# Optimization experiments

Measured on AMD Instinct MI355X. Metric: run time of the kernel, lower is better.

The kernel has to match this reference:

```python
import jax, jax.numpy as jnp
from jax import lax
import numpy as np

DG = 2          # deformable groups
KH = KW = 3     # kernel size
KK = KH * KW
PAD = 1


def setup_inputs() -> dict:
    key = jax.random.key(0)
    k1, k2, k3 = jax.random.split(key, 3)
    B, C, H, W = 4, 64, 128, 128
    O = 64
    x = jax.random.normal(k1, (B, C, H, W), jnp.float32)
    # original inits offset weights to 0 (degenerate: plain conv); use small random
    # weights instead so the irregular bilinear-gather path is actually exercised.
    w_off = jax.random.normal(k2, (DG * 2 * KK, C, KH, KW), jnp.float32) * 0.05
    w_def = jax.random.normal(k3, (O, C, KH, KW), jnp.float32) * (1.0 / np.sqrt(C * KK))
    return {"x": x, "w_off": w_off, "w_def": w_def}


def _deform_conv(x, w_off, w_def):
    B, C, H, W = x.shape
    O = w_def.shape[0]
    Cg = C // DG

    # offset = offset_conv(x): stride 1, pad 1, no bias -> [B, DG*2*KK, H, W]
    offset = lax.conv_general_dilated(
        x, w_off, window_strides=(1, 1), padding=((PAD, PAD), (PAD, PAD)),
        dimension_numbers=("NCHW", "OIHW", "NCHW"))
    # DCN layout: per group, per kernel tap k, channel 2k = dy, 2k+1 = dx
    off = offset.reshape(B, DG, KK, 2, H, W)

    ki, kj = jnp.meshgrid(jnp.arange(KH), jnp.arange(KW), indexing="ij")
    ki = (ki.reshape(KK) - PAD).astype(x.dtype)   # kernel row offsets -1..1
    kj = (kj.reshape(KK) - PAD).astype(x.dtype)
    hh = jnp.arange(H, dtype=x.dtype)
    ww = jnp.arange(W, dtype=x.dtype)

    # sampling positions [B, DG, KK, H, W]
    py = off[:, :, :, 0] + ki[None, None, :, None, None] + hh[None, None, None, :, None]
    px = off[:, :, :, 1] + kj[None, None, :, None, None] + ww[None, None, None, None, :]

    y0 = jnp.floor(py).astype(jnp.int32)
    x0 = jnp.floor(px).astype(jnp.int32)
    dy = py - y0.astype(x.dtype)
    dx = px - x0.astype(x.dtype)

    x_g = x.reshape(B, DG, Cg, H * W)

    def gather(yi, xi):
        # zero padding outside the image
        valid = ((yi >= 0) & (yi < H) & (xi >= 0) & (xi < W)).astype(x.dtype)
        yc = jnp.clip(yi, 0, H - 1)
        xc = jnp.clip(xi, 0, W - 1)
        idx = (yc * W + xc).reshape(B, DG, 1, KK * H * W)
        v = jnp.take_along_axis(x_g, idx, axis=3).reshape(B, DG, Cg, KK, H, W)
        return v * valid[:, :, None]  # broadcast over channel axis

    # bilinear interpolation at learned offset positions
    val = (gather(y0, x0) * ((1 - dy) * (1 - dx))[:, :, None]
           + gather(y0, x0 + 1) * ((1 - dy) * dx)[:, :, None]
           + gather(y0 + 1, x0) * (dy * (1 - dx))[:, :, None]
           + gather(y0 + 1, x0 + 1) * (dy * dx)[:, :, None])

    # weighted accumulation: conv groups = 1, channel dim = DG*Cg
    w = w_def.reshape(O, DG, Cg, KK)
    return jnp.einsum("bgckhw,ogck->bohw", val, w)


def reference(x, w_off, w_def):
    return _deform_conv(x, w_off, w_def)
```

## Files before the change

### kernel.cpp

```cpp
#include <hip/hip_runtime.h>
#include <hip/hip_bf16.h>

typedef _Float16 f16x8 __attribute__((ext_vector_type(8)));
typedef _Float16 f16x2 __attribute__((ext_vector_type(2)));
typedef float f32x4  __attribute__((ext_vector_type(4)));

#define Bn 4
#define Cn 64
#define Hn 128
#define Wn 128
#define HWn 16384

#define XT_BYTES    (Bn*HWn*Cn*2)
#define PKDEF_BYTES (18*4*64*8*2)

static __device__ __forceinline__ unsigned pk_f16(float lo, float hi) {
  union { _Float16 h[2]; unsigned u; } cv;
  cv.h[0] = (_Float16)lo; cv.h[1] = (_Float16)hi;
  return cv.u;
}

__global__ __launch_bounds__(256) void prep_all(const float* __restrict__ x,
                                                const float* __restrict__ w_off,
                                                const float* __restrict__ w_def,
                                                ushort* __restrict__ xt,
                                                ushort* __restrict__ pk_def,
                                                ushort* __restrict__ pk_off) {
  __shared__ float tile[64][68];
  const int t = threadIdx.x;
  const int blk = blockIdx.x;
  if (blk < 1024) {
    const int b = blk >> 8;
    const int pix0 = (blk & 255) * 64;
    const int y = pix0 >> 7, x0 = pix0 & 127;
    const float* xb = x + (b * Cn) * HWn + pix0;
#pragma unroll
    for (int q = 0; q < 4; ++q) {
      int idx = q * 256 + t;
      int c = idx >> 4, p4 = idx & 15;
      float4 v = *(const float4*)(xb + c * HWn + p4 * 4);
      *(float4*)&tile[c][p4 * 4] = v;
    }
    __syncthreads();
    const int p = t & 63, cg = t >> 6;
#pragma unroll
    for (int half = 0; half < 2; ++half) {
      const int seg = cg * 2 + half;
      unsigned u[4];
#pragma unroll
      for (int j = 0; j < 4; ++j)
        u[j] = pk_f16(tile[seg * 8 + 2 * j][p], tile[seg * 8 + 2 * j + 1][p]);
      uint4 v = {u[0], u[1], u[2], u[3]};
      *(uint4*)(xt + (((((b << 7) + y) << 3) + seg) * 128 + x0 + p) * 8) = v;
    }
  } else {
    const int tt = (blk - 1024) * 256 + t;
    if (tt < 4608) {
      int lane = tt & 63, oc = (tt >> 6) & 3, s = tt >> 8;
      int g = s / 9, k = s % 9;
      int o = oc * 16 + (lane & 15);
      int cb = g * 32 + (lane >> 4) * 8;
      unsigned u[4];
#pragma unroll
      for (int j = 0; j < 4; ++j)
        u[j] = pk_f16(w_def[(o * Cn + cb + 2 * j) * 9 + k],
                      w_def[(o * Cn + cb + 2 * j + 1) * 9 + k]);
      uint4 v = {u[0], u[1], u[2], u[3]};
      *(uint4*)(pk_def + tt * 8) = v;
    } else if (tt < 8064) {
      int t2 = tt - 4608;
      int lane = t2 & 63, r = t2 >> 6;
      int oc = r % 3, s = r / 3;
      int k = s >> 1, chalf = s & 1;
      int o = oc * 16 + (lane & 15);
      int cb = chalf * 32 + (lane >> 4) * 8;
      unsigned u[4];
#pragma unroll
      for (int j = 0; j < 4; ++j) {
        float lo = (o < 36) ? w_off[(o * Cn + cb + 2 * j) * 9 + k] : 0.f;
        float hi = (o < 36) ? w_off[(o * Cn + cb + 2 * j + 1) * 9 + k] : 0.f;
        u[j] = pk_f16(lo, hi);
      }
      uint4 v = {u[0], u[1], u[2], u[3]};
      *(uint4*)(pk_off + (r * 64 + lane) * 8) = v;
    }
  }
}

#define T_STRIDE (17*24*8 + 16)
__global__ __launch_bounds__(1024, 4) void deform_fused(const ushort* __restrict__ xt,
                                                        const ushort* __restrict__ pk_def,
                                                        const ushort* __restrict__ pk_off,
                                                        float* __restrict__ out) {
  __shared__ ushort tile[8 * T_STRIDE];
  __shared__ _Float16 off_lds[8][36][18];
  const int t = threadIdx.x;
  const int lane = t & 63;
  const int wid = t >> 6;
  const int pg = wid >> 1, gsel = wid & 1;
  int bid = blockIdx.x;
  bid = (bid & 7) * 64 + (bid >> 3);
  const int b  = bid >> 7;
  const int ty = (bid >> 3) & 15;
  const int tx = bid & 7;
  const int y0t = ty * 8, x0t = tx * 16;
  const int TLY = max(0, y0t - 4), THY = min(127, y0t + 12);
  const int TLX = max(0, x0t - 3), THX = min(127, x0t + 19);
  const int Hd = THY - TLY + 1, Wd = THX - TLX + 1;

  {
    const int xq = t & 31;
    const int r0 = t >> 5;
    const int nr = Hd * 8;
    for (int rr = r0; rr < nr; rr += 32) {
      const int yq = rr >> 3, seg = rr & 7;
      if (xq < Wd) {
        const ushort* src = xt + ((((b << 7) + TLY + yq) << 3) + seg) * 1024 + (TLX + xq) * 8;
        *(uint4*)&tile[seg * T_STRIDE + (yq * 24 + xq) * 8] = *(const uint4*)src;
      }
    }
  }
  __syncthreads();

  const int h = y0t + pg;
  const int p = lane & 15, kq = lane >> 4;
  const int w_ = x0t + p;
  const int pixin = (h << 7) + x0t;
  const int su = gsel * 4 + kq;
  const int colb = lane & 15;

  int pixoff[9]; bool tvalid[9];
#pragma unroll
  for (int kk = 0; kk < 9; ++kk) {
    int yk = h + kk / 3 - 1, xk = w_ + kk % 3 - 1;
    tvalid[kk] = ((unsigned)yk < 128u) && ((unsigned)xk < 128u);
    int yc = min(max(yk, 0), 127), xc = min(max(xk, 0), 127);
    pixoff[kk] = ((yc - TLY) * 24 + (xc - TLX)) * 8;
  }

  {
    f32x4 oa0 = {0,0,0,0}, oa1 = {0,0,0,0}, oa2 = {0,0,0,0};
    const f16x8* pBo = (const f16x8*)pk_off;
    f16x8 bo[2][2];
    if (gsel == 0) bo[0][0] = pBo[0*64 + lane];
    else { bo[0][0] = pBo[1*64 + lane]; bo[0][1] = pBo[2*64 + lane]; }
#pragma unroll
    for (int s = 0; s < 18; ++s) {
      if (s + 1 < 18) {
        if (gsel == 0) bo[(s + 1) & 1][0] = pBo[((s + 1)*3 + 0)*64 + lane];
        else { bo[(s + 1) & 1][0] = pBo[((s + 1)*3 + 1)*64 + lane];
               bo[(s + 1) & 1][1] = pBo[((s + 1)*3 + 2)*64 + lane]; }
      }
      const int k = s >> 1, chalf = s & 1;
      uint4 t_ = *(const uint4*)&tile[(chalf * 4 + kq) * T_STRIDE + pixoff[k]];
      if (!tvalid[k]) { t_.x = 0; t_.y = 0; t_.z = 0; t_.w = 0; }
      union { uint4 u; f16x8 v; } A; A.u = t_;
      if (gsel == 0) {
        oa0 = __builtin_amdgcn_mfma_f32_16x16x32_f16(A.v, bo[s & 1][0], oa0, 0,0,0);
      } else {
        oa1 = __builtin_amdgcn_mfma_f32_16x16x32_f16(A.v, bo[s & 1][0], oa1, 0,0,0);
        oa2 = __builtin_amdgcn_mfma_f32_16x16x32_f16(A.v, bo[s & 1][1], oa2, 0,0,0);
      }
    }
    if (gsel == 0) {
#pragma unroll
      for (int r = 0; r < 4; ++r) off_lds[pg][colb][kq * 4 + r] = (_Float16)oa0[r];
    } else {
#pragma unroll
      for (int r = 0; r < 4; ++r) {
        off_lds[pg][16 + colb][kq * 4 + r] = (_Float16)oa1[r];
        if (colb < 4) off_lds[pg][32 + colb][kq * 4 + r] = (_Float16)oa2[r];
      }
    }
  }
  __syncthreads();

  float offv[18];
#pragma unroll
  for (int j = 0; j < 18; ++j) offv[j] = (float)off_lds[pg][gsel * 18 + j][p];

  f32x4 acc0={0,0,0,0}, acc1={0,0,0,0}, acc2={0,0,0,0}, acc3={0,0,0,0};
  const f16x8* pB = (const f16x8*)pk_def;

  f16x8 bq[2][4];
  {
    const int s0 = gsel * 9;
#pragma unroll
    for (int q = 0; q < 4; ++q) bq[0][q] = pB[(s0*4 + q)*64 + lane];
  }

#pragma unroll
  for (int j = 0; j < 9; ++j) {
    if (j + 1 < 9) {
      const int s1 = gsel * 9 + j + 1;
#pragma unroll
      for (int q = 0; q < 4; ++q) bq[(j + 1) & 1][q] = pB[(s1*4 + q)*64 + lane];
    }

    const int k = j;
    float py = offv[2*j]   + (float)(h  + k / 3 - 1);
    float px = offv[2*j+1] + (float)(w_ + k % 3 - 1);
    float fy = floorf(py), fx = floorf(px);
    int y0 = (int)fy, x0 = (int)fx;
    float dy = py - fy, dx = px - fx;

    bool vy0 = (y0 >= 0) && (y0 < Hn);
    bool vy1 = (y0 >= -1) && (y0 < Hn - 1);
    bool vx0 = (x0 >= 0) && (x0 < Wn);
    bool vx1 = (x0 >= -1) && (x0 < Wn - 1);
    float omdy = 1.f - dy, omdx = 1.f - dx;
    float w00 = (vy0 && vx0) ? omdy * omdx : 0.f;
    float w01 = (vy0 && vx1) ? omdy * dx   : 0.f;
    float w10 = (vy1 && vx0) ? dy * omdx   : 0.f;
    float w11 = (vy1 && vx1) ? dy * dx     : 0.f;

    int iy0 = min(max(y0, 0), Hn - 1), iy1 = min(max(y0 + 1, 0), Hn - 1);
    int ix0 = min(max(x0, 0), Wn - 1), ix1 = min(max(x0 + 1, 0), Wn - 1);

    uint4 c00, c01, c10, c11;
    bool intile = (iy0 >= TLY) && (iy1 <= THY) && (ix0 >= TLX) && (ix1 <= THX);
    if (__all((int)intile)) {
      const int base = su * T_STRIDE;
      const int ly0 = iy0 - TLY, ly1 = iy1 - TLY;
      const int lx0 = ix0 - TLX, lx1 = ix1 - TLX;
      c00 = *(const uint4*)&tile[base + (ly0 * 24 + lx0) * 8];
      c01 = *(const uint4*)&tile[base + (ly0 * 24 + lx1) * 8];
      c10 = *(const uint4*)&tile[base + (ly1 * 24 + lx0) * 8];
      c11 = *(const uint4*)&tile[base + (ly1 * 24 + lx1) * 8];
    } else {
      const int r0g = ((((b << 7) + iy0) << 3) + su) * 128;
      const int r1g = ((((b << 7) + iy1) << 3) + su) * 128;
      c00 = *(const uint4*)(xt + (r0g + ix0) * 8);
      c01 = *(const uint4*)(xt + (r0g + ix1) * 8);
      c10 = *(const uint4*)(xt + (r1g + ix0) * 8);
      c11 = *(const uint4*)(xt + (r1g + ix1) * 8);
    }

    const _Float16 h00 = (_Float16)w00, h01 = (_Float16)w01;
    const _Float16 h10 = (_Float16)w10, h11 = (_Float16)w11;
    const f16x2 W00 = {h00, h00}, W01 = {h01, h01};
    const f16x2 W10 = {h10, h10}, W11 = {h11, h11};
    union U32H { unsigned u; f16x2 h; };
    union { uint4 u; f16x8 v; } A;
#define BILC(comp, fld)                                                        \
    { U32H a0, a1, a2, a3, r;                                                  \
      a0.u = c00.comp; a1.u = c01.comp; a2.u = c10.comp; a3.u = c11.comp;      \
      r.h = a0.h * W00 + a1.h * W01 + a2.h * W10 + a3.h * W11;                 \
      A.u.fld = r.u; }
    BILC(x, x) BILC(y, y) BILC(z, z) BILC(w, w)
#undef BILC

    acc0 = __builtin_amdgcn_mfma_f32_16x16x32_f16(A.v, bq[j & 1][0], acc0, 0,0,0);
    acc1 = __builtin_amdgcn_mfma_f32_16x16x32_f16(A.v, bq[j & 1][1], acc1, 0,0,0);
    acc2 = __builtin_amdgcn_mfma_f32_16x16x32_f16(A.v, bq[j & 1][2], acc2, 0,0,0);
    acc3 = __builtin_amdgcn_mfma_f32_16x16x32_f16(A.v, bq[j & 1][3], acc3, 0,0,0);
  }

  __syncthreads();
  float* red = (float*)tile;
  if (gsel == 1) {
    *(f32x4*)&red[((pg * 4 + 0) * 64 + lane) * 4] = acc0;
    *(f32x4*)&red[((pg * 4 + 1) * 64 + lane) * 4] = acc1;
  } else {
    *(f32x4*)&red[((pg * 4 + 2) * 64 + lane) * 4] = acc2;
    *(f32x4*)&red[((pg * 4 + 3) * 64 + lane) * 4] = acc3;
  }
  __syncthreads();
  float* ob = out + pixin + kq * 4;
  if (gsel == 0) {
    acc0 += *(const f32x4*)&red[((pg * 4 + 0) * 64 + lane) * 4];
    acc1 += *(const f32x4*)&red[((pg * 4 + 1) * 64 + lane) * 4];
#pragma unroll
    for (int r = 0; r < 4; ++r) {
      ob[((b*64 +      colb) << 14) + r] = acc0[r];
      ob[((b*64 + 16 + colb) << 14) + r] = acc1[r];
    }
  } else {
    acc2 += *(const f32x4*)&red[((pg * 4 + 2) * 64 + lane) * 4];
    acc3 += *(const f32x4*)&red[((pg * 4 + 3) * 64 + lane) * 4];
#pragma unroll
    for (int r = 0; r < 4; ++r) {
      ob[((b*64 + 32 + colb) << 14) + r] = acc2[r];
      ob[((b*64 + 48 + colb) << 14) + r] = acc3[r];
    }
  }
}

extern "C" void kernel_launch(void* const* d_in, const int* in_sizes, int n_in,
                              void* d_out, int out_size, void* d_ws, size_t ws_size,
                              hipStream_t stream) {
  const float* x     = (const float*)d_in[0];
  const float* w_off = (const float*)d_in[1];
  const float* w_def = (const float*)d_in[2];
  float* out = (float*)d_out;

  char* ws = (char*)d_ws;
  ushort* xt     = (ushort*)ws;
  ushort* pk_def = (ushort*)(ws + XT_BYTES);
  ushort* pk_off = (ushort*)(ws + XT_BYTES + PKDEF_BYTES);

  prep_all<<<1056, 256, 0, stream>>>(x, w_off, w_def, xt, pk_def, pk_off);
  deform_fused<<<512, 1024, 0, stream>>>(xt, pk_def, pk_off, out);
}
```

Measured before the change: 55.00 us.

## Process two row tiles per block with double-buffered async LDS staging

Each block now handles two vertically adjacent 8-row tiles, halving the grid. The second tile's halo is staged into a second LDS buffer with global_load_lds while the first tile's bilinear/MFMA phase runs. The intent is to hide tile-load latency behind compute and reuse per-block setup. The cost is fewer blocks and more LDS per block, which may reduce parallelism on a 256-CU device.

```diff
diff --git a/kernel.cpp b/kernel.cpp
--- a/kernel.cpp
+++ b/kernel.cpp
@@ -14,10 +14,19 @@
 #define XT_BYTES    (Bn*HWn*Cn*2)
 #define PKDEF_BYTES (18*4*64*8*2)
 
+#define T_STRIDE (17*25*8)
+#define TILE_USH (8*T_STRIDE)
+
 static __device__ __forceinline__ unsigned pk_f16(float lo, float hi) {
   union { _Float16 h[2]; unsigned u; } cv;
   cv.h[0] = (_Float16)lo; cv.h[1] = (_Float16)hi;
   return cv.u;
+}
+
+static __device__ __forceinline__ void gload16(const ushort* g, ushort* l) {
+  __builtin_amdgcn_global_load_lds(
+      (const __attribute__((address_space(1))) void*)g,
+      (__attribute__((address_space(3))) void*)l, 16, 0, 0);
 }
 
 __global__ __launch_bounds__(256) void prep_all(const float* __restrict__ x,
@@ -87,60 +96,62 @@
   }
 }
 
-#define T_STRIDE (17*24*8 + 16)
 __global__ __launch_bounds__(1024, 4) void deform_fused(const ushort* __restrict__ xt,
                                                         const ushort* __restrict__ pk_def,
                                                         const ushort* __restrict__ pk_off,
                                                         float* __restrict__ out) {
-  __shared__ ushort tile[8 * T_STRIDE];
+  __shared__ __align__(16) ushort tA[TILE_USH];
+  __shared__ __align__(16) ushort tB[TILE_USH];
   __shared__ _Float16 off_lds[8][36][18];
   const int t = threadIdx.x;
   const int lane = t & 63;
   const int wid = t >> 6;
   const int pg = wid >> 1, gsel = wid & 1;
   int bid = blockIdx.x;
-  bid = (bid & 7) * 64 + (bid >> 3);
-  const int b  = bid >> 7;
-  const int ty = (bid >> 3) & 15;
-  const int tx = bid & 7;
-  const int y0t = ty * 8, x0t = tx * 16;
-  const int TLY = max(0, y0t - 4), THY = min(127, y0t + 12);
-  const int TLX = max(0, x0t - 3), THX = min(127, x0t + 19);
-  const int Hd = THY - TLY + 1, Wd = THX - TLX + 1;
-
-  {
-    const int xq = t & 31;
-    const int r0 = t >> 5;
-    const int nr = Hd * 8;
-    for (int rr = r0; rr < nr; rr += 32) {
-      const int yq = rr >> 3, seg = rr & 7;
-      if (xq < Wd) {
-        const ushort* src = xt + ((((b << 7) + TLY + yq) << 3) + seg) * 1024 + (TLX + xq) * 8;
-        *(uint4*)&tile[seg * T_STRIDE + (yq * 24 + xq) * 8] = *(const uint4*)src;
-      }
-    }
-  }
-  __syncthreads();
-
-  const int h = y0t + pg;
+  bid = (bid & 7) * 32 + (bid >> 3);
+  const int b   = bid >> 6;
+  const int typ = (bid >> 3) & 7;
+  const int tx  = bid & 7;
+  const int x0t = tx * 16;
+
   const int p = lane & 15, kq = lane >> 4;
   const int w_ = x0t + p;
-  const int pixin = (h << 7) + x0t;
   const int su = gsel * 4 + kq;
   const int colb = lane & 15;
-
-  int pixoff[9]; bool tvalid[9];
-#pragma unroll
-  for (int kk = 0; kk < 9; ++kk) {
-    int yk = h + kk / 3 - 1, xk = w_ + kk % 3 - 1;
-    tvalid[kk] = ((unsigned)yk < 128u) && ((unsigned)xk < 128u);
-    int yc = min(max(yk, 0), 127), xc = min(max(xk, 0), 127);
-    pixoff[kk] = ((yc - TLY) * 24 + (xc - TLX)) * 8;
-  }
-
-  {
+  const f16x8* pB  = (const f16x8*)pk_def;
+  const f16x8* pBo = (const f16x8*)pk_off;
+
+  auto stage = [&](ushort* tbuf, int y0t) {
+    const int TLY = max(0, y0t - 4);
+    const int TLX = max(0, x0t - 4);
+    for (int base = wid * 64; base < 3400; base += 1024) {
+      int fi = base + lane;
+      if (fi < 3400) {
+        int seg = fi / 425;
+        int r   = fi - seg * 425;
+        int yq  = r / 25;
+        int xq  = r - yq * 25;
+        int gy = min(TLY + yq, 127);
+        int gx = min(TLX + xq, 127);
+        const ushort* src = xt + ((((b << 7) + gy) << 3) + seg) * 1024 + gx * 8;
+        gload16(src, tbuf + base * 8);
+      }
+    }
+  };
+
+  auto P1 = [&](const ushort* tbuf, int y0t) {
+    const int TLY = max(0, y0t - 4);
+    const int TLX = max(0, x0t - 4);
+    const int h = y0t + pg;
+    int pixoff[9]; bool tvalid[9];
+#pragma unroll
+    for (int kk = 0; kk < 9; ++kk) {
+      int yk = h + kk / 3 - 1, xk = w_ + kk % 3 - 1;
+      tvalid[kk] = ((unsigned)yk < 128u) && ((unsigned)xk < 128u);
+      int yc = min(max(yk, 0), 127), xc = min(max(xk, 0), 127);
+      pixoff[kk] = ((yc - TLY) * 25 + (xc - TLX)) * 8;
+    }
     f32x4 oa0 = {0,0,0,0}, oa1 = {0,0,0,0}, oa2 = {0,0,0,0};
-    const f16x8* pBo = (const f16x8*)pk_off;
     f16x8 bo[2][2];
     if (gsel == 0) bo[0][0] = pBo[0*64 + lane];
     else { bo[0][0] = pBo[1*64 + lane]; bo[0][1] = pBo[2*64 + lane]; }
@@ -152,7 +163,7 @@
                bo[(s + 1) & 1][1] = pBo[((s + 1)*3 + 2)*64 + lane]; }
       }
       const int k = s >> 1, chalf = s & 1;
-      uint4 t_ = *(const uint4*)&tile[(chalf * 4 + kq) * T_STRIDE + pixoff[k]];
+      uint4 t_ = *(const uint4*)&tbuf[(chalf * 4 + kq) * T_STRIDE + pixoff[k]];
       if (!tvalid[k]) { t_.x = 0; t_.y = 0; t_.z = 0; t_.w = 0; }
       union { uint4 u; f16x8 v; } A; A.u = t_;
       if (gsel == 0) {
@@ -172,118 +183,135 @@
         if (colb < 4) off_lds[pg][32 + colb][kq * 4 + r] = (_Float16)oa2[r];
       }
     }
-  }
-  __syncthreads();
-
-  float offv[18];
-#pragma unroll
-  for (int j = 0; j < 18; ++j) offv[j] = (float)off_lds[pg][gsel * 18 + j][p];
-
-  f32x4 acc0={0,0,0,0}, acc1={0,0,0,0}, acc2={0,0,0,0}, acc3={0,0,0,0};
-  const f16x8* pB = (const f16x8*)pk_def;
-
-  f16x8 bq[2][4];
-  {
-    const int s0 = gsel * 9;
-#pragma unroll
-    for (int q = 0; q < 4; ++q) bq[0][q] = pB[(s0*4 + q)*64 + lane];
-  }
-
-#pragma unroll
-  for (int j = 0; j < 9; ++j) {
-    if (j + 1 < 9) {
-      const int s1 = gsel * 9 + j + 1;
-#pragma unroll
-      for (int q = 0; q < 4; ++q) bq[(j + 1) & 1][q] = pB[(s1*4 + q)*64 + lane];
-    }
-
-    const int k = j;
-    float py = offv[2*j]   + (float)(h  + k / 3 - 1);
-    float px = offv[2*j+1] + (float)(w_ + k % 3 - 1);
-    float fy = floorf(py), fx = floorf(px);
-    int y0 = (int)fy, x0 = (int)fx;
-    float dy = py - fy, dx = px - fx;
-
-    bool vy0 = (y0 >= 0) && (y0 < Hn);
-    bool vy1 = (y0 >= -1) && (y0 < Hn - 1);
-    bool vx0 = (x0 >= 0) && (x0 < Wn);
-    bool vx1 = (x0 >= -1) && (x0 < Wn - 1);
-    float omdy = 1.f - dy, omdx = 1.f - dx;
-    float w00 = (vy0 && vx0) ? omdy * omdx : 0.f;
-    float w01 = (vy0 && vx1) ? omdy * dx   : 0.f;
-    float w10 = (vy1 && vx0) ? dy * omdx   : 0.f;
-    float w11 = (vy1 && vx1) ? dy * dx     : 0.f;
-
-    int iy0 = min(max(y0, 0), Hn - 1), iy1 = min(max(y0 + 1, 0), Hn - 1);
-    int ix0 = min(max(x0, 0), Wn - 1), ix1 = min(max(x0 + 1, 0), Wn - 1);
-
-    uint4 c00, c01, c10, c11;
-    bool intile = (iy0 >= TLY) && (iy1 <= THY) && (ix0 >= TLX) && (ix1 <= THX);
-    if (__all((int)intile)) {
-      const int base = su * T_STRIDE;
-      const int ly0 = iy0 - TLY, ly1 = iy1 - TLY;
-      const int lx0 = ix0 - TLX, lx1 = ix1 - TLX;
-      c00 = *(const uint4*)&tile[base + (ly0 * 24 + lx0) * 8];
-      c01 = *(const uint4*)&tile[base + (ly0 * 24 + lx1) * 8];
-      c10 = *(const uint4*)&tile[base + (ly1 * 24 + lx0) * 8];
-      c11 = *(const uint4*)&tile[base + (ly1 * 24 + lx1) * 8];
+  };
+
+  f32x4 acc0, acc1, acc2, acc3;
+
+  auto P2 = [&](const ushort* tbuf, int y0t) {
+    const int TLY = max(0, y0t - 4), THY = min(127, y0t + 12);
+    const int TLX = max(0, x0t - 4), THX = min(127, x0t + 20);
+    const int h = y0t + pg;
+    float offv[18];
+#pragma unroll
+    for (int j = 0; j < 18; ++j) offv[j] = (float)off_lds[pg][gsel * 18 + j][p];
+    acc0 = (f32x4){0,0,0,0}; acc1 = (f32x4){0,0,0,0};
+    acc2 = (f32x4){0,0,0,0}; acc3 = (f32x4){0,0,0,0};
+    f16x8 bq[2][4];
+    {
+      const int s0 = gsel * 9;
+#pragma unroll
+      for (int q = 0; q < 4; ++q) bq[0][q] = pB[(s0*4 + q)*64 + lane];
+    }
+#pragma unroll
+    for (int j = 0; j < 9; ++j) {
+      if (j + 1 < 9) {
+        const int s1 = gsel * 9 + j + 1;
+#pragma unroll
+        for (int q = 0; q < 4; ++q) bq[(j + 1) & 1][q] = pB[(s1*4 + q)*64 + lane];
+      }
+      const int k = j;
+      float py = offv[2*j]   + (float)(h  + k / 3 - 1);
+      float px = offv[2*j+1] + (float)(w_ + k % 3 - 1);
+      float fy = floorf(py), fx = floorf(px);
+      int y0 = (int)fy, x0 = (int)fx;
+      float dy = py - fy, dx = px - fx;
+      bool vy0 = (y0 >= 0) && (y0 < Hn);
+      bool vy1 = (y0 >= -1) && (y0 < Hn - 1);
+      bool vx0 = (x0 >= 0) && (x0 < Wn);
+      bool vx1 = (x0 >= -1) && (x0 < Wn - 1);
+      float omdy = 1.f - dy, omdx = 1.f - dx;
+      float w00 = (vy0 && vx0) ? omdy * omdx : 0.f;
+      float w01 = (vy0 && vx1) ? omdy * dx   : 0.f;
+      float w10 = (vy1 && vx0) ? dy * omdx   : 0.f;
+      float w11 = (vy1 && vx1) ? dy * dx     : 0.f;
+      int iy0 = min(max(y0, 0), Hn - 1), iy1 = min(max(y0 + 1, 0), Hn - 1);
+      int ix0 = min(max(x0, 0), Wn - 1), ix1 = min(max(x0 + 1, 0), Wn - 1);
+      uint4 c00, c01, c10, c11;
+      bool intile = (iy0 >= TLY) && (iy1 <= THY) && (ix0 >= TLX) && (ix1 <= THX);
+      if (__all((int)intile)) {
+        const int base = su * T_STRIDE;
+        const int ly0 = iy0 - TLY, ly1 = iy1 - TLY;
+        const int lx0 = ix0 - TLX, lx1 = ix1 - TLX;
+        c00 = *(const uint4*)&tbuf[base + (ly0 * 25 + lx0) * 8];
+        c01 = *(const uint4*)&tbuf[base + (ly0 * 25 + lx1) * 8];
+        c10 = *(const uint4*)&tbuf[base + (ly1 * 25 + lx0) * 8];
+        c11 = *(const uint4*)&tbuf[base + (ly1 * 25 + lx1) * 8];
+      } else {
+        const int r0g = ((((b << 7) + iy0) << 3) + su) * 128;
+        const int r1g = ((((b << 7) + iy1) << 3) + su) * 128;
+        c00 = *(const uint4*)(xt + (r0g + ix0) * 8);
+        c01 = *(const uint4*)(xt + (r0g + ix1) * 8);
+        c10 = *(const uint4*)(xt + (r1g + ix0) * 8);
+        c11 = *(const uint4*)(xt + (r1g + ix1) * 8);
+      }
+      const _Float16 h00 = (_Float16)w00, h01 = (_Float16)w01;
+      const _Float16 h10 = (_Float16)w10, h11 = (_Float16)w11;
+      const f16x2 W00 = {h00, h00}, W01 = {h01, h01};
+      const f16x2 W10 = {h10, h10}, W11 = {h11, h11};
+      union U32H { unsigned u; f16x2 h; };
+      union { uint4 u; f16x8 v; } A;
+#define BILC(comp, fld)                                                        \
+      { U32H a0, a1, a2, a3, r;                                                \
+        a0.u = c00.comp; a1.u = c01.comp; a2.u = c10.comp; a3.u = c11.comp;    \
+        r.h = a0.h * W00 + a1.h * W01 + a2.h * W10 + a3.h * W11;               \
+        A.u.fld = r.u; }
+      BILC(x, x) BILC(y, y) BILC(z, z) BILC(w, w)
+#undef BILC
+      acc0 = __builtin_amdgcn_mfma_f32_16x16x32_f16(A.v, bq[j & 1][0], acc0, 0,0,0);
+      acc1 = __builtin_amdgcn_mfma_f32_16x16x32_f16(A.v, bq[j & 1][1], acc1, 0,0,0);
+      acc2 = __builtin_amdgcn_mfma_f32_16x16x32_f16(A.v, bq[j & 1][2], acc2, 0,0,0);
+      acc3 = __builtin_amdgcn_mfma_f32_16x16x32_f16(A.v, bq[j & 1][3], acc3, 0,0,0);
+    }
+  };
+
+  auto RW = [&](float* red, int y0t) {
+    const int h = y0t + pg;
+    const int pixin = (h << 7) + x0t;
+    if (gsel == 1) {
+      *(f32x4*)&red[((pg * 4 + 0) * 64 + lane) * 4] = acc0;
+      *(f32x4*)&red[((pg * 4 + 1) * 64 + lane) * 4] = acc1;
     } else {
-      const int r0g = ((((b << 7) + iy0) << 3) + su) * 128;
-      const int r1g = ((((b << 7) + iy1) << 3) + su) * 128;
-      c00 = *(const uint4*)(xt + (r0g + ix0) * 8);
-      c01 = *(const uint4*)(xt + (r0g + ix1) * 8);
-      c10 = *(const uint4*)(xt + (r1g + ix0) * 8);
-      c11 = *(const uint4*)(xt + (r1g + ix1) * 8);
-    }
-
-    const _Float16 h00 = (_Float16)w00, h01 = (_Float16)w01;
-    const _Float16 h10 = (_Float16)w10, h11 = (_Float16)w11;
-    const f16x2 W00 = {h00, h00}, W01 = {h01, h01};
-    const f16x2 W10 = {h10, h10}, W11 = {h11, h11};
-    union U32H { unsigned u; f16x2 h; };
-    union { uint4 u; f16x8 v; } A;
-#define BILC(comp, fld)                                                        \
-    { U32H a0, a1, a2, a3, r;                                                  \
-      a0.u = c00.comp; a1.u = c01.comp; a2.u = c10.comp; a3.u = c11.comp;      \
-      r.h = a0.h * W00 + a1.h * W01 + a2.h * W10 + a3.h * W11;                 \
-      A.u.fld = r.u; }
-    BILC(x, x) BILC(y, y) BILC(z, z) BILC(w, w)
-#undef BILC
-
-    acc0 = __builtin_amdgcn_mfma_f32_16x16x32_f16(A.v, bq[j & 1][0], acc0, 0,0,0);
-    acc1 = __builtin_amdgcn_mfma_f32_16x16x32_f16(A.v, bq[j & 1][1], acc1, 0,0,0);
-    acc2 = __builtin_amdgcn_mfma_f32_16x16x32_f16(A.v, bq[j & 1][2], acc2, 0,0,0);
-    acc3 = __builtin_amdgcn_mfma_f32_16x16x32_f16(A.v, bq[j & 1][3], acc3, 0,0,0);
-  }
-
-  __syncthreads();
-  float* red = (float*)tile;
-  if (gsel == 1) {
-    *(f32x4*)&red[((pg * 4 + 0) * 64 + lane) * 4] = acc0;
-    *(f32x4*)&red[((pg * 4 + 1) * 64 + lane) * 4] = acc1;
-  } else {
-    *(f32x4*)&red[((pg * 4 + 2) * 64 + lane) * 4] = acc2;
-    *(f32x4*)&red[((pg * 4 + 3) * 64 + lane) * 4] = acc3;
-  }
-  __syncthreads();
-  float* ob = out + pixin + kq * 4;
-  if (gsel == 0) {
-    acc0 += *(const f32x4*)&red[((pg * 4 + 0) * 64 + lane) * 4];
-    acc1 += *(const f32x4*)&red[((pg * 4 + 1) * 64 + lane) * 4];
-#pragma unroll
-    for (int r = 0; r < 4; ++r) {
-      ob[((b*64 +      colb) << 14) + r] = acc0[r];
-      ob[((b*64 + 16 + colb) << 14) + r] = acc1[r];
-    }
-  } else {
-    acc2 += *(const f32x4*)&red[((pg * 4 + 2) * 64 + lane) * 4];
-    acc3 += *(const f32x4*)&red[((pg * 4 + 3) * 64 + lane) * 4];
-#pragma unroll
-    for (int r = 0; r < 4; ++r) {
-      ob[((b*64 + 32 + colb) << 14) + r] = acc2[r];
-      ob[((b*64 + 48 + colb) << 14) + r] = acc3[r];
-    }
-  }
+      *(f32x4*)&red[((pg * 4 + 2) * 64 + lane) * 4] = acc2;
+      *(f32x4*)&red[((pg * 4 + 3) * 64 + lane) * 4] = acc3;
+    }
+    __syncthreads();
+    float* ob = out + pixin + kq * 4;
+    if (gsel == 0) {
+      acc0 += *(const f32x4*)&red[((pg * 4 + 0) * 64 + lane) * 4];
+      acc1 += *(const f32x4*)&red[((pg * 4 + 1) * 64 + lane) * 4];
+#pragma unroll
+      for (int r = 0; r < 4; ++r) {
+        ob[((b*64 +      colb) << 14) + r] = acc0[r];
+        ob[((b*64 + 16 + colb) << 14) + r] = acc1[r];
+      }
+    } else {
+      acc2 += *(const f32x4*)&red[((pg * 4 + 2) * 64 + lane) * 4];
+      acc3 += *(const f32x4*)&red[((pg * 4 + 3) * 64 + lane) * 4];
+#pragma unroll
+      for (int r = 0; r < 4; ++r) {
+        ob[((b*64 + 32 + colb) << 14) + r] = acc2[r];
+        ob[((b*64 + 48 + colb) << 14) + r] = acc3[r];
+      }
+    }
+  };
+
+  const int y0t0 = typ * 16;
+  const int y0t1 = typ * 16 + 8;
+
+  stage(tA, y0t0);
+  __syncthreads();
+  P1(tA, y0t0);
+  __syncthreads();
+  stage(tB, y0t1);
+  P2(tA, y0t0);
+  __syncthreads();
+  RW((float*)tA, y0t0);
+  __syncthreads();
+  P1(tB, y0t1);
+  __syncthreads();
+  P2(tB, y0t1);
+  __syncthreads();
+  RW((float*)tB, y0t1);
 }
 
 extern "C" void kernel_launch(void* const* d_in, const int* in_sizes, int n_in,
@@ -300,5 +328,5 @@
   ushort* pk_off = (ushort*)(ws + XT_BYTES + PKDEF_BYTES);
 
   prep_all<<<1056, 256, 0, stream>>>(x, w_off, w_def, xt, pk_def, pk_off);
-  deform_fused<<<512, 1024, 0, stream>>>(xt, pk_def, pk_off, out);
-}
+  deform_fused<<<256, 1024, 0, stream>>>(xt, pk_def, pk_off, out);
+}
```

Measured after the change: 58.22 us. 1.06x slower.
